# Performance work log

Measured on AMD Instinct MI355X. Metric: run time of the kernel, lower is better.

## Reference

```python
import jax, jax.numpy as jnp
import numpy as np
import math

N_HEADS = 4


def setup_inputs() -> dict:
    key = jax.random.key(0)
    k1, k2, k3 = jax.random.split(key, 3)
    B, C, T = 4096, 256, 64
    q = jax.random.normal(k1, (B, C, 1), dtype=jnp.float32)
    k = jax.random.normal(k2, (B, C, T), dtype=jnp.float32)
    v = jax.random.normal(k3, (B, C, T), dtype=jnp.float32)
    return {"q": q, "k": k, "v": v,
            "use_gumbel_softmax": 1, "is_train": 0, "hard_mode": 0}


def reference(q, k, v, use_gumbel_softmax, is_train, hard_mode):
    bs, width, length = k.shape
    assert k.shape == v.shape
    assert width % N_HEADS == 0
    ch = width // N_HEADS
    scale = 1.0 / math.sqrt(math.sqrt(ch))

    qh = (q * scale).reshape(bs * N_HEADS, ch, -1)   # [BH, ch, 1]
    kh = (k * scale).reshape(bs * N_HEADS, ch, -1)   # [BH, ch, T]
    vh = v.reshape(bs * N_HEADS, ch, -1)             # [BH, ch, T]

    # [BH, 1, T] attention logits; stable softmax in fp32 then cast back
    weight = jnp.einsum('bct,bcs->bts', qh, kh)
    weight = jax.nn.softmax(weight.astype(jnp.float32), axis=-1).astype(weight.dtype)

    if use_gumbel_softmax:
        # eval path (is_train=False): deterministic argmax one-hot selection
        weight_onehot = (weight == jnp.max(weight, axis=-1, keepdims=True)).astype(jnp.float32)
        weight = weight * weight_onehot
        a = jnp.einsum('bts,bcs->bct', weight_onehot, vh)   # [BH, ch, 1]
    else:
        a = jnp.einsum('bts,bcs->bct', weight, vh)

    weight_sum = jnp.sum(weight, axis=2, keepdims=True)     # [BH, 1, 1]
    if N_HEADS > 1:
        weight_sum = weight_sum.reshape(bs, N_HEADS, -1)
        weight_sum = jnp.sum(weight_sum, axis=1, keepdims=True)  # [B, 1, 1]

    return a.reshape(bs, width, -1), weight_sum
```

## Files before the change

### kernel.cpp

```cpp
#include <hip/hip_runtime.h>
#include <cstdint>


__global__ __launch_bounds__(256) void qkv_gumbel_attn(
    const float* __restrict__ q,
    const float* __restrict__ k,
    const float* __restrict__ v,
    float* __restrict__ out_a,
    float* __restrict__ out_ws)
{
    constexpr float SCALE = 0.35355339059327373f;
    const int b   = blockIdx.x;
    const int tid = threadIdx.x;
    const int h   = tid >> 6;
    const int l   = tid & 63;

    __shared__ float sq[256];
    __shared__ float sws[4];

    sq[tid] = q[(size_t)b * 256 + tid] * SCALE;
    __syncthreads();

    const int r = l >> 4;
    const float4* __restrict__ k4 = reinterpret_cast<const float4*>(k);
    const size_t kbase = (size_t)b * 4096 + (size_t)h * 1024;

    float a0 = 0.f, a1 = 0.f, a2 = 0.f, a3 = 0.f;
#pragma unroll
    for (int i = 0; i < 16; ++i) {
        const float  qc = sq[h * 64 + 4 * i + r];
        const float4 kv = k4[kbase + (size_t)(i * 64 + l)];
        a0 = fmaf(qc, kv.x * SCALE, a0);
        a1 = fmaf(qc, kv.y * SCALE, a1);
        a2 = fmaf(qc, kv.z * SCALE, a2);
        a3 = fmaf(qc, kv.w * SCALE, a3);
    }
    a0 += __shfl_xor(a0, 16); a0 += __shfl_xor(a0, 32);
    a1 += __shfl_xor(a1, 16); a1 += __shfl_xor(a1, 32);
    a2 += __shfl_xor(a2, 16); a2 += __shfl_xor(a2, 32);
    a3 += __shfl_xor(a3, 16); a3 += __shfl_xor(a3, 32);

    float m = fmaxf(fmaxf(a0, a1), fmaxf(a2, a3));
#pragma unroll
    for (int off = 1; off <= 8; off <<= 1) m = fmaxf(m, __shfl_xor(m, off));

    const float e0 = expf(a0 - m), e1 = expf(a1 - m),
                e2 = expf(a2 - m), e3 = expf(a3 - m);
    float d = e0 + e1 + e2 + e3;
#pragma unroll
    for (int off = 1; off <= 8; off <<= 1) d += __shfl_xor(d, off);

    const float p0 = e0 / d, p1 = e1 / d, p2 = e2 / d, p3 = e3 / d;
    float pm = fmaxf(fmaxf(p0, p1), fmaxf(p2, p3));
#pragma unroll
    for (int off = 1; off <= 8; off <<= 1) pm = fmaxf(pm, __shfl_xor(pm, off));

    uint64_t m0 = __ballot(p0 == pm) & 0xFFFFull;
    uint64_t m1 = __ballot(p1 == pm) & 0xFFFFull;
    uint64_t m2 = __ballot(p2 == pm) & 0xFFFFull;
    uint64_t m3 = __ballot(p3 == pm) & 0xFFFFull;

    const int cnt = __popcll(m0) + __popcll(m1) + __popcll(m2) + __popcll(m3);

    const float* __restrict__ vrow =
        v + (size_t)b * 16384 + (size_t)(h * 64 + l) * 64;
    float aval = 0.f;
    while (m0) { int i2 = __ffsll((unsigned long long)m0) - 1; m0 &= m0 - 1; aval += vrow[4 * i2 + 0]; }
    while (m1) { int i2 = __ffsll((unsigned long long)m1) - 1; m1 &= m1 - 1; aval += vrow[4 * i2 + 1]; }
    while (m2) { int i2 = __ffsll((unsigned long long)m2) - 1; m2 &= m2 - 1; aval += vrow[4 * i2 + 2]; }
    while (m3) { int i2 = __ffsll((unsigned long long)m3) - 1; m3 &= m3 - 1; aval += vrow[4 * i2 + 3]; }

    out_a[(size_t)b * 256 + tid] = aval;

    if (l == 0) sws[h] = pm * (float)cnt;
    __syncthreads();
    if (tid == 0) out_ws[b] = ((sws[0] + sws[1]) + sws[2]) + sws[3];
}

extern "C" void kernel_launch(void* const* d_in, const int* in_sizes, int n_in,
                              void* d_out, int out_size, void* d_ws, size_t ws_size,
                              hipStream_t stream) {
    const float* q = (const float*)d_in[0];
    const float* k = (const float*)d_in[1];
    const float* v = (const float*)d_in[2];
    float* out_a  = (float*)d_out;
    float* out_ws = out_a + (size_t)4096 * 256;
    qkv_gumbel_attn<<<dim3(4096), dim3(256), 0, stream>>>(q, k, v, out_a, out_ws);
}
```

Baseline: 79.33 us.

## Stream K through double-buffered LDS via async global_load_lds and simplify argmax

Replaces the direct float4 global loads of K with asynchronous global-to-LDS copies into a per-wave double buffer, issuing the next chunk's loads before consuming the current one. The goal is to keep more memory requests in flight and hide load latency behind the dot-product FMAs. It also computes the softmax max directly as 1/d instead of a separate shuffle reduction over the probabilities, and sets a minimum occupancy hint in launch bounds. The 32 KB of LDS per block may limit occupancy. The block barrier after writing sq is replaced by a compiler-only fence, which is only safe because each wave reads only its own slice of sq.

```diff
diff --git a/kernel.cpp b/kernel.cpp
--- a/kernel.cpp
+++ b/kernel.cpp
@@ -2,7 +2,10 @@
 #include <cstdint>
 
 
-__global__ __launch_bounds__(256) void qkv_gumbel_attn(
+typedef __attribute__((address_space(3))) void lds_t;
+typedef const __attribute__((address_space(1))) void glb_t;
+
+__global__ __launch_bounds__(256, 4) void qkv_gumbel_attn(
     const float* __restrict__ q,
     const float* __restrict__ k,
     const float* __restrict__ v,
@@ -14,27 +17,51 @@
     const int tid = threadIdx.x;
     const int h   = tid >> 6;
     const int l   = tid & 63;
+    const int r4  = l >> 4;
 
+    __shared__ float sk[4][2][1024];
     __shared__ float sq[256];
     __shared__ float sws[4];
 
     sq[tid] = q[(size_t)b * 256 + tid] * SCALE;
-    __syncthreads();
+    asm volatile("" ::: "memory");
 
-    const int r = l >> 4;
-    const float4* __restrict__ k4 = reinterpret_cast<const float4*>(k);
-    const size_t kbase = (size_t)b * 4096 + (size_t)h * 1024;
+    const float4* __restrict__ k4 =
+        reinterpret_cast<const float4*>(k) + (size_t)b * 4096 + (size_t)h * 1024;
+
+#pragma unroll
+    for (int i = 0; i < 4; ++i) {
+        __builtin_amdgcn_global_load_lds((glb_t*)(k4 + i * 64 + l),
+                                         (lds_t*)&sk[h][0][i * 256], 16, 0, 0);
+    }
 
     float a0 = 0.f, a1 = 0.f, a2 = 0.f, a3 = 0.f;
 #pragma unroll
-    for (int i = 0; i < 16; ++i) {
-        const float  qc = sq[h * 64 + 4 * i + r];
-        const float4 kv = k4[kbase + (size_t)(i * 64 + l)];
-        a0 = fmaf(qc, kv.x * SCALE, a0);
-        a1 = fmaf(qc, kv.y * SCALE, a1);
-        a2 = fmaf(qc, kv.z * SCALE, a2);
-        a3 = fmaf(qc, kv.w * SCALE, a3);
+    for (int r = 0; r < 4; ++r) {
+        if (r < 3) {
+#pragma unroll
+            for (int i = 0; i < 4; ++i) {
+                __builtin_amdgcn_global_load_lds(
+                    (glb_t*)(k4 + (r + 1) * 256 + i * 64 + l),
+                    (lds_t*)&sk[h][(r + 1) & 1][i * 256], 16, 0, 0);
+            }
+            asm volatile("s_waitcnt vmcnt(4)" ::: "memory");
+        } else {
+            asm volatile("s_waitcnt vmcnt(0)" ::: "memory");
+        }
+        const float* __restrict__ buf = sk[h][r & 1];
+#pragma unroll
+        for (int i = 0; i < 4; ++i) {
+            const float4 kv =
+                *reinterpret_cast<const float4*>(&buf[i * 256 + 4 * l]);
+            const float qc = sq[h * 64 + r * 16 + 4 * i + r4];
+            a0 = fmaf(qc, kv.x * SCALE, a0);
+            a1 = fmaf(qc, kv.y * SCALE, a1);
+            a2 = fmaf(qc, kv.z * SCALE, a2);
+            a3 = fmaf(qc, kv.w * SCALE, a3);
+        }
     }
+
     a0 += __shfl_xor(a0, 16); a0 += __shfl_xor(a0, 32);
     a1 += __shfl_xor(a1, 16); a1 += __shfl_xor(a1, 32);
     a2 += __shfl_xor(a2, 16); a2 += __shfl_xor(a2, 32);
@@ -50,25 +77,22 @@
 #pragma unroll
     for (int off = 1; off <= 8; off <<= 1) d += __shfl_xor(d, off);
 
-    const float p0 = e0 / d, p1 = e1 / d, p2 = e2 / d, p3 = e3 / d;
-    float pm = fmaxf(fmaxf(p0, p1), fmaxf(p2, p3));
-#pragma unroll
-    for (int off = 1; off <= 8; off <<= 1) pm = fmaxf(pm, __shfl_xor(pm, off));
+    const float pm = 1.0f / d;
 
-    uint64_t m0 = __ballot(p0 == pm) & 0xFFFFull;
-    uint64_t m1 = __ballot(p1 == pm) & 0xFFFFull;
-    uint64_t m2 = __ballot(p2 == pm) & 0xFFFFull;
-    uint64_t m3 = __ballot(p3 == pm) & 0xFFFFull;
+    uint64_t m0 = __ballot(e0 / d == pm) & 0xFFFFull;
+    uint64_t m1 = __ballot(e1 / d == pm) & 0xFFFFull;
+    uint64_t m2 = __ballot(e2 / d == pm) & 0xFFFFull;
+    uint64_t m3 = __ballot(e3 / d == pm) & 0xFFFFull;
 
     const int cnt = __popcll(m0) + __popcll(m1) + __popcll(m2) + __popcll(m3);
 
     const float* __restrict__ vrow =
         v + (size_t)b * 16384 + (size_t)(h * 64 + l) * 64;
     float aval = 0.f;
-    while (m0) { int i2 = __ffsll((unsigned long long)m0) - 1; m0 &= m0 - 1; aval += vrow[4 * i2 + 0]; }
-    while (m1) { int i2 = __ffsll((unsigned long long)m1) - 1; m1 &= m1 - 1; aval += vrow[4 * i2 + 1]; }
-    while (m2) { int i2 = __ffsll((unsigned long long)m2) - 1; m2 &= m2 - 1; aval += vrow[4 * i2 + 2]; }
-    while (m3) { int i2 = __ffsll((unsigned long long)m3) - 1; m3 &= m3 - 1; aval += vrow[4 * i2 + 3]; }
+    while (m0) { int s = __ffsll((unsigned long long)m0) - 1; m0 &= m0 - 1; aval += vrow[4 * s + 0]; }
+    while (m1) { int s = __ffsll((unsigned long long)m1) - 1; m1 &= m1 - 1; aval += vrow[4 * s + 1]; }
+    while (m2) { int s = __ffsll((unsigned long long)m2) - 1; m2 &= m2 - 1; aval += vrow[4 * s + 2]; }
+    while (m3) { int s = __ffsll((unsigned long long)m3) - 1; m3 &= m3 - 1; aval += vrow[4 * s + 3]; }
 
     out_a[(size_t)b * 256 + tid] = aval;
 
```

Result: faster. 77.12 us (-2.8%).

## Split fused attention into logits/mask kernel and separate V gather kernel

Applied to the files above, without the earlier changes.

Splits the single fused kernel into two launches. The first computes logits, softmax and argmax masks and writes a 64-bit mask per head into workspace. The second reads the masks and gathers V. It also computes the max probability as 1/d instead of doing a shuffle reduction. The aim is to shorten the dependent gather latency inside the first kernel, but it adds a second launch and a workspace round-trip, and the gather still reads strided, uncoalesced V elements.

```diff
diff --git a/kernel.cpp b/kernel.cpp
--- a/kernel.cpp
+++ b/kernel.cpp
@@ -2,18 +2,18 @@
 #include <cstdint>
 
 
-__global__ __launch_bounds__(256) void qkv_gumbel_attn(
+__global__ __launch_bounds__(256) void qkv_phase1_logits(
     const float* __restrict__ q,
     const float* __restrict__ k,
-    const float* __restrict__ v,
-    float* __restrict__ out_a,
-    float* __restrict__ out_ws)
+    float* __restrict__ out_ws,
+    unsigned long long* __restrict__ masks)
 {
     constexpr float SCALE = 0.35355339059327373f;
     const int b   = blockIdx.x;
     const int tid = threadIdx.x;
     const int h   = tid >> 6;
     const int l   = tid & 63;
+    const int r4  = l >> 4;
 
     __shared__ float sq[256];
     __shared__ float sws[4];
@@ -21,14 +21,13 @@
     sq[tid] = q[(size_t)b * 256 + tid] * SCALE;
     __syncthreads();
 
-    const int r = l >> 4;
     const float4* __restrict__ k4 = reinterpret_cast<const float4*>(k);
     const size_t kbase = (size_t)b * 4096 + (size_t)h * 1024;
 
     float a0 = 0.f, a1 = 0.f, a2 = 0.f, a3 = 0.f;
 #pragma unroll
     for (int i = 0; i < 16; ++i) {
-        const float  qc = sq[h * 64 + 4 * i + r];
+        const float  qc = sq[h * 64 + 4 * i + r4];
         const float4 kv = k4[kbase + (size_t)(i * 64 + l)];
         a0 = fmaf(qc, kv.x * SCALE, a0);
         a1 = fmaf(qc, kv.y * SCALE, a1);
@@ -50,31 +49,45 @@
 #pragma unroll
     for (int off = 1; off <= 8; off <<= 1) d += __shfl_xor(d, off);
 
-    const float p0 = e0 / d, p1 = e1 / d, p2 = e2 / d, p3 = e3 / d;
-    float pm = fmaxf(fmaxf(p0, p1), fmaxf(p2, p3));
-#pragma unroll
-    for (int off = 1; off <= 8; off <<= 1) pm = fmaxf(pm, __shfl_xor(pm, off));
+    const float pm = 1.0f / d;
 
-    uint64_t m0 = __ballot(p0 == pm) & 0xFFFFull;
-    uint64_t m1 = __ballot(p1 == pm) & 0xFFFFull;
-    uint64_t m2 = __ballot(p2 == pm) & 0xFFFFull;
-    uint64_t m3 = __ballot(p3 == pm) & 0xFFFFull;
+    const uint64_t m0 = __ballot(e0 / d == pm) & 0xFFFFull;
+    const uint64_t m1 = __ballot(e1 / d == pm) & 0xFFFFull;
+    const uint64_t m2 = __ballot(e2 / d == pm) & 0xFFFFull;
+    const uint64_t m3 = __ballot(e3 / d == pm) & 0xFFFFull;
+    const uint64_t mm = m0 | (m1 << 16) | (m2 << 32) | (m3 << 48);
+    const int cnt = __popcll((unsigned long long)mm);
 
-    const int cnt = __popcll(m0) + __popcll(m1) + __popcll(m2) + __popcll(m3);
+    if (l == 0) {
+        masks[(size_t)b * 4 + h] = mm;
+        sws[h] = pm * (float)cnt;
+    }
+    __syncthreads();
+    if (tid == 0) out_ws[b] = ((sws[0] + sws[1]) + sws[2]) + sws[3];
+}
+
+__global__ __launch_bounds__(256) void qkv_phase2_gather(
+    const float* __restrict__ v,
+    const unsigned long long* __restrict__ masks,
+    float* __restrict__ out_a)
+{
+    const int b   = blockIdx.x;
+    const int tid = threadIdx.x;
+    const int h   = tid >> 6;
+    const int l   = tid & 63;
+
+    uint64_t mm = masks[(size_t)b * 4 + h];
 
     const float* __restrict__ vrow =
         v + (size_t)b * 16384 + (size_t)(h * 64 + l) * 64;
-    float aval = 0.f;
-    while (m0) { int i2 = __ffsll((unsigned long long)m0) - 1; m0 &= m0 - 1; aval += vrow[4 * i2 + 0]; }
-    while (m1) { int i2 = __ffsll((unsigned long long)m1) - 1; m1 &= m1 - 1; aval += vrow[4 * i2 + 1]; }
-    while (m2) { int i2 = __ffsll((unsigned long long)m2) - 1; m2 &= m2 - 1; aval += vrow[4 * i2 + 2]; }
-    while (m3) { int i2 = __ffsll((unsigned long long)m3) - 1; m3 &= m3 - 1; aval += vrow[4 * i2 + 3]; }
 
-    out_a[(size_t)b * 256 + tid] = aval;
-
-    if (l == 0) sws[h] = pm * (float)cnt;
-    __syncthreads();
-    if (tid == 0) out_ws[b] = ((sws[0] + sws[1]) + sws[2]) + sws[3];
+    float a = 0.f;
+    while (mm) {
+        const int bit = __ffsll((unsigned long long)mm) - 1;
+        mm &= mm - 1;
+        a += vrow[4 * (bit & 15) + (bit >> 4)];
+    }
+    out_a[(size_t)b * 256 + tid] = a;
 }
 
 extern "C" void kernel_launch(void* const* d_in, const int* in_sizes, int n_in,
@@ -85,5 +98,8 @@
     const float* v = (const float*)d_in[2];
     float* out_a  = (float*)d_out;
     float* out_ws = out_a + (size_t)4096 * 256;
-    qkv_gumbel_attn<<<dim3(4096), dim3(256), 0, stream>>>(q, k, v, out_a, out_ws);
+    unsigned long long* masks = (unsigned long long*)d_ws;
+
+    qkv_phase1_logits<<<dim3(4096), dim3(256), 0, stream>>>(q, k, out_ws, masks);
+    qkv_phase2_gather<<<dim3(4096), dim3(256), 0, stream>>>(v, masks, out_a);
 }
```

Measured after the change: 78.89 us. About the same (-0.6%).
